# Kernel optimization log

Hardware: AMD Instinct MI355X
Metric: run time of the kernel (lower is better)

The kernel has to match this reference:

```python
import jax, jax.numpy as jnp
import numpy as np

B_, N, C, H = 512, 49, 256, 8
DH = C // H            # 32
RB, NRF = 8, 32
NWIN = B_ // RB        # 64
DC = 64                # class_token_dim
TC = C + 2 * DC        # 384
WS = 7
SCALE = DH ** -0.5


def _rel_pos_index():
    ch = np.arange(WS)
    coords = np.stack(np.meshgrid(ch, ch, indexing='ij')).reshape(2, -1)  # [2,49]
    rel = (coords[:, :, None] - coords[:, None, :]).transpose(1, 2, 0)    # [49,49,2]
    rel[..., 0] += WS - 1
    rel[..., 1] += WS - 1
    rel[..., 0] *= 2 * WS - 1
    return jnp.asarray(rel.sum(-1).reshape(-1))  # [49*49]


def _ln(x, axes, eps=1e-5):
    m = x.mean(axes, keepdims=True)
    v = x.var(axes, keepdims=True)
    return (x - m) * jax.lax.rsqrt(v + eps)


def setup_inputs() -> dict:
    key = jax.random.key(0)
    ks = jax.random.split(key, 20)
    def w(i, shape, s=0.02):
        return jax.random.normal(ks[i], shape, jnp.float32) * s
    return dict(
        x=w(0, (B_, N, C), 1.0),
        x_ref=w(1, (RB, NRF, C), 1.0),
        depth_token=w(2, (B_, N, DC), 1.0),
        seg_token=w(3, (B_, N, DC), 1.0),
        qkv_w=w(4, (C, 3 * C)), qkv_b=jnp.zeros(3 * C, jnp.float32),
        proj_w=w(5, (C, C)), proj_b=jnp.zeros(C, jnp.float32),
        rel_bias=w(6, ((2 * WS - 1) ** 2, H)),
        diff_mu=w(7, (1, 1, C), 1.0), diff_logsigma=w(8, (1, 1, C)),
        ref_qk_w=w(9, (C, 2 * C)), ref_qk_b=jnp.zeros(2 * C, jnp.float32),
        conv_w=w(10, (H, H, 3, 3), 0.1), conv_b=jnp.zeros(H, jnp.float32),
        q_norm_w=jnp.ones(C, jnp.float32), q_norm_b=jnp.zeros(C, jnp.float32),
        q_proj_w=w(11, (C, C)), q_proj_b=jnp.zeros(C, jnp.float32),
        cls_dth_q_w=w(12, (DC, DC)), cls_dth_q_b=jnp.zeros(DC, jnp.float32),
        cls_seg_q_w=w(13, (DC, DC)), cls_seg_q_b=jnp.zeros(DC, jnp.float32),
        global_k_w=w(14, (TC, TC)), global_k_b=jnp.zeros(TC, jnp.float32),
        global_v_w=w(15, (TC, TC)), global_v_b=jnp.zeros(TC, jnp.float32),
        proj_dth_w=w(16, (DC, DC)), proj_dth_b=jnp.zeros(DC, jnp.float32),
    )


def reference(x, x_ref, depth_token, seg_token, qkv_w, qkv_b, proj_w, proj_b,
              rel_bias, diff_mu, diff_logsigma, ref_qk_w, ref_qk_b, conv_w, conv_b,
              q_norm_w, q_norm_b, q_proj_w, q_proj_b, cls_dth_q_w, cls_dth_q_b,
              cls_seg_q_w, cls_seg_q_b, global_k_w, global_k_b, global_v_w,
              global_v_b, proj_dth_w, proj_dth_b):
    # qkv: [B_,N,3C] -> q,k,v each [B_,H,N,DH]
    qkv = (x @ qkv_w + qkv_b).reshape(B_, N, 3, H, DH).transpose(2, 0, 3, 1, 4)
    q, k, v = qkv[0], qkv[1], qkv[2]

    # ---- group attention (ref branch) ----
    ref_qk = (x_ref @ ref_qk_w + ref_qk_b).reshape(RB, NRF, 2, C).transpose(2, 0, 1, 3)
    ref_q, ref_v = ref_qk[0], ref_qk[1]                       # [RB,NRF,C]
    ref_q = diff_mu + jnp.exp(diff_logsigma) * ref_q
    ref_q = ref_q.reshape(RB, NRF, H, DH).transpose(0, 2, 1, 3)  # [RB,H,NRF,DH]
    ref_v = ref_v.reshape(RB, NRF, H, DH).transpose(0, 2, 1, 3)

    qs = (q * SCALE).reshape(RB, NWIN, H, N, DH)
    # scores against shared (per-image) ref keys; avoids materializing repeated K
    ref_attn = jnp.einsum('rwhnd,rhfd->rhwnf', qs, ref_q)     # [RB,H,NWIN,N,NRF]
    ref_attn_r = ref_attn.reshape(RB, H, NWIN * N, NRF)
    # 3-step diffusion: conv2d over heads-as-channels + LN(no affine) + gelu, residual
    for _ in range(3):
        u = jax.lax.conv_general_dilated(
            ref_attn_r, conv_w, (1, 1), 'SAME',
            dimension_numbers=('NCHW', 'OIHW', 'NCHW')) + conv_b[None, :, None, None]
        u = jax.nn.gelu(_ln(u, (-2, -1)), approximate=False)
        ref_attn_r = ref_attn_r + u
    ref_attn = jax.nn.softmax(ref_attn_r.reshape(RB, H, NWIN, N, NRF), axis=-1)
    q_new = jnp.einsum('rhwnf,rhfd->rwnhd', ref_attn, ref_v).reshape(B_, N, C)
    q_sc = q.transpose(0, 2, 1, 3).reshape(B_, N, C)          # unscaled shortcut
    q_new = (_ln(q_new + q_sc, (-1,)) * q_norm_w + q_norm_b) @ q_proj_w + q_proj_b + q_sc
    q_new = q_new.reshape(B_, N, H, DH).transpose(0, 2, 1, 3) * SCALE

    # ---- window attention with relative position bias ----
    bias = rel_bias[_rel_pos_index()].reshape(N, N, H).transpose(2, 0, 1)  # [H,N,N]
    attn = jax.nn.softmax(jnp.einsum('bhnd,bhmd->bhnm', q_new, k) + bias[None], axis=-1)
    out = jnp.einsum('bhnm,bhmd->bnhd', attn, v).reshape(B_, N, C)
    out = out @ proj_w + proj_b

    # ---- class-token global attention ----
    dch = DC // H   # 8
    tdh = TC // H   # 48
    depth_q = (depth_token @ cls_dth_q_w + cls_dth_q_b).reshape(B_, N, H, dch).transpose(0, 2, 1, 3) * SCALE
    seg_q = (seg_token @ cls_seg_q_w + cls_seg_q_b).reshape(B_, N, H, dch).transpose(0, 2, 1, 3) * SCALE
    t_x = jnp.concatenate([out, depth_token, seg_token], axis=-1)  # [B_,N,TC]
    t_k = (t_x @ global_k_w + global_k_b).reshape(B_, N, H, tdh).transpose(0, 2, 1, 3)
    t_v = (t_x @ global_v_w + global_v_b).reshape(B_, N, H, tdh).transpose(0, 2, 1, 3)

    d_attn = jax.nn.softmax(jnp.einsum('bhnc,bhnt->bhct', depth_q, t_k), axis=-1)
    d_tok = jnp.einsum('bhct,bhnt->bhcn', d_attn, t_v).reshape(B_, DC, N).transpose(0, 2, 1)
    d_tok = d_tok @ proj_dth_w + proj_dth_b
    s_attn = jax.nn.softmax(jnp.einsum('bhnc,bhnt->bhct', seg_q, t_k), axis=-1)
    s_tok = jnp.einsum('bhct,bhnt->bhcn', s_attn, t_v).reshape(B_, DC, N).transpose(0, 2, 1)
    s_tok = s_tok @ proj_dth_w + proj_dth_b  # NOTE: original uses proj_dth for seg too
    return out, d_tok, s_tok
```

## Files before the change

kernel.cpp:

```cpp
#include <hip/hip_runtime.h>
#include <hip/hip_bf16.h>

typedef __hip_bfloat16 bf16;
typedef short s16x8 __attribute__((ext_vector_type(8)));
typedef float f32x4 __attribute__((ext_vector_type(4)));
union V16 { uint4 u4; s16x8 s8; unsigned u[4]; unsigned short s[8]; };

static __device__ __forceinline__ float b2f(bf16 v){ return __bfloat162float(v); }
static __device__ __forceinline__ bf16  f2b(float v){ return __float2bfloat16(v); }
static __device__ __forceinline__ unsigned short f2bs(float x){
    union { float f; unsigned u; } c; c.f = x;
    unsigned r = c.u + 0x7fff + ((c.u >> 16) & 1);
    return (unsigned short)(r >> 16);
}
static __device__ __forceinline__ float bu2f(unsigned short b){
    union { unsigned u; float f; } c; c.u = ((unsigned)b) << 16; return c.f;
}
static __device__ __forceinline__ s16x8 ld16g(const bf16* p){
    V16 u; u.u4 = *(const uint4*)p; return u.s8;
}
static __device__ __forceinline__ void glds16(const void* g, void* l){
    __builtin_amdgcn_global_load_lds(
        (const __attribute__((address_space(1))) unsigned*)g,
        (__attribute__((address_space(3))) unsigned*)l, 16, 0, 0);
}

#define SCALE_T 0.17677669529663687f

__global__ __launch_bounds__(256) void prep_weights(
    const float* __restrict__ qkvw, const float* __restrict__ qpw,
    const float* __restrict__ pw,   const float* __restrict__ gkw,
    const float* __restrict__ gvw,  bf16* __restrict__ Wt)
{
    int idx = blockIdx.x * 256 + threadIdx.x;
    float v;
    if (idx < 196608)      { int j = idx;          int n = j >> 8, k = j & 255; v = qkvw[k * 768 + n]; }
    else if (idx < 262144) { int j = idx - 196608; int n = j >> 8, k = j & 255; v = qpw[k * 256 + n]; }
    else if (idx < 327680) { int j = idx - 262144; int n = j >> 8, k = j & 255; v = pw[k * 256 + n]; }
    else if (idx < 475136) { int j = idx - 327680; int n = j / 384, k = j - n * 384; v = gkw[k * 384 + n]; }
    else                   { int j = idx - 475136; int n = j / 384, k = j - n * 384; v = gvw[k * 384 + n]; }
    ((unsigned short*)Wt)[idx] = f2bs(v);
}

__global__ __launch_bounds__(256, 2) void gemm128(
    const void* __restrict__ A, int akind, int lda,
    const float* __restrict__ tokD, const float* __restrict__ tokS,
    const bf16* __restrict__ Wt, const float* __restrict__ bias,
    const float* __restrict__ bias2,
    const bf16* __restrict__ addp, int addStride,
    float* __restrict__ outF, bf16* __restrict__ outB, int outStrideB,
    int M, int K, int N, float scale)
{
    __shared__ char lds[2][16384];

    const int tid = threadIdx.x;
    const int wv = tid >> 6, lane = tid & 63;
    const int quad = lane >> 4, l15 = lane & 15;
    const int wr = wv >> 1, wc = wv & 1;

    const int gx = (int)gridDim.x;
    const int nwg = gx * (int)gridDim.y;
    int bid = (int)blockIdx.y * gx + (int)blockIdx.x;
    if ((nwg & 7) == 0) bid = (bid & 7) * (nwg >> 3) + (bid >> 3);
    const int bx = bid % gx, by = bid / gx;
    const int rowBase = by * 128, colBase = bx * 128;

    const int srow = tid >> 2;
    const int kOff = (((tid & 3) ^ (srow & 3)) << 3);

    const unsigned swz = (unsigned)((quad ^ (l15 & 3)) << 4);
    const unsigned aoff0 = (unsigned)(wr * 4096 + l15 * 64) + swz;
    const unsigned boff0 = (unsigned)(wc * 4096 + l15 * 64) + swz;

    f32x4 acc[4][4];
    #pragma unroll
    for (int m = 0; m < 4; ++m)
        #pragma unroll
        for (int n = 0; n < 4; ++n)
            #pragma unroll
            for (int r = 0; r < 4; ++r) acc[m][n][r] = 0.f;

    const bf16*  Ab = (const bf16*)A;
    const float* Af = (const float*)A;

    auto stage = [&](int sbuf, int kt) {
        char* base = &lds[sbuf][0];
        #pragma unroll
        for (int c = 0; c < 2; ++c) {
            const bf16* src = Wt + (size_t)(colBase + c * 64 + srow) * K + (kt + kOff);
            glds16(src, base + 8192 + c * 4096 + tid * 16);
        }
        if (akind == 0) {
            #pragma unroll
            for (int c = 0; c < 2; ++c) {
                const bf16* src = Ab + (size_t)(rowBase + c * 64 + srow) * lda + (kt + kOff);
                glds16(src, base + c * 4096 + tid * 16);
            }
        } else {
            #pragma unroll
            for (int c = 0; c < 2; ++c) {
                int row = rowBase + c * 64 + srow;
                const float* src;
                if (akind == 1) {
                    src = Af + (size_t)row * lda + (kt + kOff);
                } else {
                    if (kt < 256)      src = Af   + (size_t)row * 256 + (kt + kOff);
                    else if (kt < 320) src = tokD + (size_t)row * 64  + (kt - 256 + kOff);
                    else               src = tokS + (size_t)row * 64  + (kt - 320 + kOff);
                }
                float4 u0 = ((const float4*)src)[0];
                float4 u1 = ((const float4*)src)[1];
                V16 o;
                o.s[0] = f2bs(u0.x); o.s[1] = f2bs(u0.y);
                o.s[2] = f2bs(u0.z); o.s[3] = f2bs(u0.w);
                o.s[4] = f2bs(u1.x); o.s[5] = f2bs(u1.y);
                o.s[6] = f2bs(u1.z); o.s[7] = f2bs(u1.w);
                *(uint4*)(base + c * 4096 + tid * 16) = o.u4;
            }
        }
    };

    stage(0, 0);
    __syncthreads();
    int buf = 0;
    for (int kt = 0; kt < K; kt += 32) {
        if (kt + 32 < K) stage(buf ^ 1, kt + 32);
        const char* Abase = &lds[buf][0];
        const char* Bbase = Abase + 8192;
        s16x8 af[4], bfr[4];
        #pragma unroll
        for (int m = 0; m < 4; ++m) af[m]  = *(const s16x8*)(Abase + aoff0 + m * 1024);
        #pragma unroll
        for (int n = 0; n < 4; ++n) bfr[n] = *(const s16x8*)(Bbase + boff0 + n * 1024);
        #pragma unroll
        for (int m = 0; m < 4; ++m)
            #pragma unroll
            for (int n = 0; n < 4; ++n)
                acc[m][n] = __builtin_amdgcn_mfma_f32_16x16x32_bf16(af[m], bfr[n], acc[m][n], 0, 0, 0);
        __syncthreads();
        buf ^= 1;
    }

    #pragma unroll
    for (int n = 0; n < 4; ++n) {
        int col = colBase + wc * 64 + n * 16 + l15;
        float bb = bias2 ? (col < 384 ? bias[col] : bias2[col - 384]) : bias[col];
        #pragma unroll
        for (int m = 0; m < 4; ++m) {
            #pragma unroll
            for (int r = 0; r < 4; ++r) {
                int row = rowBase + wr * 64 + m * 16 + quad * 4 + r;
                float v = acc[m][n][r] + bb;
                if (addp) v += b2f(addp[(size_t)row * addStride + col]);
                v *= scale;
                if (outF) outF[(size_t)row * N + col] = v;
                if (outB) outB[(size_t)row * outStrideB + col] = f2b(v);
            }
        }
    }
}

__global__ __launch_bounds__(256) void mfma_gemm(
    const void* __restrict__ A, int a_mode,
    const float* __restrict__ Xd, const float* __restrict__ Xs,
    const float* __restrict__ W, const float* __restrict__ bias,
    const bf16* __restrict__ addp, int addStride,
    float* __restrict__ outF, bf16* __restrict__ outB,
    int M, int K, int N, float scale)
{
    __shared__ __hip_bfloat16 Al[64][48];
    __shared__ __hip_bfloat16 Bl[64][48];

    const int tid  = threadIdx.x;
    const int wv   = tid >> 6, lane = tid & 63;
    const int quad = lane >> 4, l15 = lane & 15;
    const int rowBase = blockIdx.y * 64, colBase = blockIdx.x * 64;

    const int am = tid >> 2, ak = (tid & 3) * 8;
    const int bn = tid & 63, bk = (tid >> 6) * 8;

    f32x4 acc[4];
    #pragma unroll
    for (int t = 0; t < 4; ++t)
        #pragma unroll
        for (int r = 0; r < 4; ++r) acc[t][r] = 0.f;

    for (int kt = 0; kt < K; kt += 32) {
        s16x8 sa;
        if (a_mode == 1) {
            const bf16* Ab = (const bf16*)A;
            V16 u; u.u4 = *(const uint4*)(Ab + (size_t)(rowBase + am) * K + kt + ak);
            sa = u.s8;
        } else {
            const float* src; size_t base;
            if (a_mode == 0) {
                src = (const float*)A; base = (size_t)(rowBase + am) * K + kt + ak;
            } else {
                int kcol = kt + ak;
                if (kcol < 256)      { src = (const float*)A; base = (size_t)(rowBase + am) * 256 + kcol; }
                else if (kcol < 320) { src = Xd; base = (size_t)(rowBase + am) * 64 + (kcol - 256); }
                else                 { src = Xs; base = (size_t)(rowBase + am) * 64 + (kcol - 320); }
            }
            const float4* p = (const float4*)(src + base);
            float4 u0 = p[0], u1 = p[1];
            sa[0] = (short)f2bs(u0.x); sa[1] = (short)f2bs(u0.y);
            sa[2] = (short)f2bs(u0.z); sa[3] = (short)f2bs(u0.w);
            sa[4] = (short)f2bs(u1.x); sa[5] = (short)f2bs(u1.y);
            sa[6] = (short)f2bs(u1.z); sa[7] = (short)f2bs(u1.w);
        }
        *(s16x8*)&Al[am][ak] = sa;

        s16x8 sb;
        #pragma unroll
        for (int j = 0; j < 8; ++j)
            sb[j] = (short)f2bs(W[(size_t)(kt + bk + j) * N + colBase + bn]);
        *(s16x8*)&Bl[bn][bk] = sb;

        __syncthreads();

        s16x8 a = *(const s16x8*)&Al[wv * 16 + l15][quad * 8];
        #pragma unroll
        for (int t = 0; t < 4; ++t) {
            s16x8 b = *(const s16x8*)&Bl[t * 16 + l15][quad * 8];
            acc[t] = __builtin_amdgcn_mfma_f32_16x16x32_bf16(a, b, acc[t], 0, 0, 0);
        }
        __syncthreads();
    }

    #pragma unroll
    for (int t = 0; t < 4; ++t) {
        int col = colBase + t * 16 + l15;
        float bb = bias[col];
        #pragma unroll
        for (int r = 0; r < 4; ++r) {
            int row = rowBase + wv * 16 + quad * 4 + r;
            float v = acc[t][r] + bb;
            if (addp) v += b2f(addp[(size_t)row * addStride + col]);
            v *= scale;
            if (outF) outF[(size_t)row * N + col] = v;
            if (outB) outB[(size_t)row * N + col] = f2b(v);
        }
    }
}

__global__ __launch_bounds__(256) void refprep_kernel(
    const float* __restrict__ ref_qk, const float* __restrict__ mu,
    const float* __restrict__ ls, float* __restrict__ ref_q_t,
    float* __restrict__ ref_v_t)
{
    int idx = blockIdx.x * 256 + threadIdx.x;
    int d = idx & 31, f = (idx >> 5) & 31, h = (idx >> 10) & 7, r = idx >> 13;
    int c = h * 32 + d;
    size_t src = (size_t)(r * 32 + f) * 512 + c;
    ref_q_t[idx] = mu[c] + __expf(ls[c]) * ref_qk[src];
    ref_v_t[idx] = ref_qk[src + 256];
}

__global__ __launch_bounds__(256) void refattn_kernel(
    const bf16* __restrict__ qkv, const float* __restrict__ ref_q_t,
    bf16* __restrict__ ref_attn)
{
    int blk = blockIdx.x;
    int w = blk & 63, h = (blk >> 6) & 7, r = blk >> 9;
    int b = r * 64 + w;
    __shared__ float qt[49 * 32];
    __shared__ float rq[32 * 33];
    int tid = threadIdx.x;
    for (int l = tid; l < 1568; l += 256) {
        int n = l >> 5, d = l & 31;
        qt[l] = b2f(qkv[(size_t)(b * 49 + n) * 768 + h * 32 + d]) * SCALE_T;
    }
    for (int l = tid; l < 1024; l += 256) {
        int f = l >> 5, d = l & 31;
        rq[f * 33 + d] = ref_q_t[(size_t)((r * 8 + h) * 32 + f) * 32 + d];
    }
    __syncthreads();
    for (int l = tid; l < 1568; l += 256) {
        int n = l >> 5, f = l & 31;
        float acc = 0.f;
        #pragma unroll
        for (int d2 = 0; d2 < 32; ++d2) acc += qt[n * 32 + d2] * rq[f * 33 + d2];
        ref_attn[(size_t)(((r * 8 + h) * 64 + w) * 49 + n) * 32 + f] = f2b(acc);
    }
}

__global__ __launch_bounds__(256) void conv_kernel(
    const bf16* __restrict__ in, const float* __restrict__ conv_w,
    const float* __restrict__ conv_b, bf16* __restrict__ u)
{
    __shared__ float w_s[576];
    __shared__ float b_s[8];
    int tid = threadIdx.x;
    for (int l = tid; l < 576; l += 256) w_s[l] = conv_w[l];
    if (tid < 8) b_s[tid] = conv_b[tid];
    __syncthreads();

    int idx = blockIdx.x * 256 + tid;
    int fb = idx & 3;
    int p  = (idx >> 2) % 3136;
    int r  = idx / 12544;
    int f0 = fb * 8;

    float acc[8][8];
    #pragma unroll
    for (int o = 0; o < 8; ++o) {
        float bo = b_s[o];
        #pragma unroll
        for (int f = 0; f < 8; ++f) acc[o][f] = bo;
    }

    for (int i = 0; i < 8; ++i) {
        float ext[3][10];
        #pragma unroll
        for (int dy = 0; dy < 3; ++dy) {
            int pp = p + dy - 1;
            bool pv = (unsigned)pp < 3136u;
            size_t base = ((size_t)((r * 8 + i) * 3136 + (pv ? pp : 0))) * 32 + f0;
            V16 uv;
            uv.u4 = pv ? *(const uint4*)(in + base) : make_uint4(0, 0, 0, 0);
            #pragma unroll
            for (int j = 0; j < 8; ++j) {
                unsigned sh = uv.u[j >> 1];
                unsigned bits = (j & 1) ? (sh & 0xffff0000u) : (sh << 16);
                union { unsigned uu; float fl; } cv; cv.uu = bits;
                ext[dy][j + 1] = cv.fl;
            }
            ext[dy][0] = (pv && f0 > 0)      ? b2f(in[base - 1]) : 0.f;
            ext[dy][9] = (pv && f0 + 8 < 32) ? b2f(in[base + 8]) : 0.f;
        }
        #pragma unroll
        for (int o = 0; o < 8; ++o) {
            #pragma unroll
            for (int ky = 0; ky < 3; ++ky) {
                const float* wp = &w_s[((o * 8 + i) * 3 + ky) * 3];
                float w0 = wp[0], w1 = wp[1], w2 = wp[2];
                #pragma unroll
                for (int f = 0; f < 8; ++f)
                    acc[o][f] += ext[ky][f] * w0 + ext[ky][f + 1] * w1 + ext[ky][f + 2] * w2;
            }
        }
    }

    #pragma unroll
    for (int o = 0; o < 8; ++o) {
        bf16 ov[8];
        #pragma unroll
        for (int f = 0; f < 8; ++f) ov[f] = f2b(acc[o][f]);
        *(uint4*)(u + ((size_t)((r * 8 + o) * 3136 + p)) * 32 + f0) = *(uint4*)ov;
    }
}

__global__ __launch_bounds__(256) void lnstats_kernel(
    const bf16* __restrict__ u, float* __restrict__ stats)
{
    int g = blockIdx.x;
    const bf16* p = u + (size_t)g * 100352;
    int tid = threadIdx.x;
    float s = 0.f, s2 = 0.f;
    for (int it = tid; it < 12544; it += 256) {
        V16 uv; uv.u4 = *(const uint4*)(p + it * 8);
        #pragma unroll
        for (int j = 0; j < 8; ++j) {
            unsigned sh = uv.u[j >> 1];
            unsigned bits = (j & 1) ? (sh & 0xffff0000u) : (sh << 16);
            union { unsigned uu; float fl; } cv; cv.uu = bits;
            s += cv.fl; s2 += cv.fl * cv.fl;
        }
    }
    __shared__ float r1[256], r2[256];
    r1[tid] = s; r2[tid] = s2; __syncthreads();
    for (int st = 128; st > 0; st >>= 1) {
        if (tid < st) { r1[tid] += r1[tid + st]; r2[tid] += r2[tid + st]; }
        __syncthreads();
    }
    if (tid == 0) {
        float mean = r1[0] * (1.f / 100352.f);
        float var  = r2[0] * (1.f / 100352.f) - mean * mean;
        var = fmaxf(var, 0.f);
        stats[g * 2] = mean;
        stats[g * 2 + 1] = rsqrtf(var + 1e-5f);
    }
}

__global__ __launch_bounds__(256) void lngelu_kernel(
    const bf16* __restrict__ u, const float* __restrict__ stats,
    bf16* __restrict__ ref_attn)
{
    int idx8 = blockIdx.x * 256 + threadIdx.x;
    int g = idx8 / 12544;
    size_t base = (size_t)idx8 * 8;
    float mean = stats[g * 2], rstd = stats[g * 2 + 1];
    V16 uv; uv.u4 = *(const uint4*)(u + base);
    V16 rv; rv.u4 = *(const uint4*)(ref_attn + base);
    bf16 outv[8];
    #pragma unroll
    for (int j = 0; j < 8; ++j) {
        unsigned shu = uv.u[j >> 1];
        unsigned shr = rv.u[j >> 1];
        unsigned bu = (j & 1) ? (shu & 0xffff0000u) : (shu << 16);
        unsigned br = (j & 1) ? (shr & 0xffff0000u) : (shr << 16);
        union { unsigned uu; float fl; } cu, cr; cu.uu = bu; cr.uu = br;
        float v = (cu.fl - mean) * rstd;
        float ge = 0.5f * v * (1.f + erff(v * 0.7071067811865476f));
        outv[j] = f2b(cr.fl + ge);
    }
    *(uint4*)(ref_attn + base) = *(uint4*)outv;
}

__global__ __launch_bounds__(256) void qnew_pre_kernel(
    const bf16* __restrict__ qkv, const bf16* __restrict__ ref_attn,
    const float* __restrict__ ref_v_t,
    const float* __restrict__ qnw, const float* __restrict__ qnb,
    bf16* __restrict__ ln_t)
{
    int ww = threadIdx.x >> 6, lane = threadIdx.x & 63;
    int row = blockIdx.x * 4 + ww;
    int b = row / 49, n = row % 49;
    int r = b >> 6, w = b & 63;
    int h = lane >> 3, d0 = (lane & 7) * 4;

    const bf16* la = ref_attn + ((size_t)(((r * 8 + h) * 64 + w) * 49 + n)) * 32 + d0;
    ushort4 lu = *(const ushort4*)la;
    float lg[4] = { bu2f(lu.x), bu2f(lu.y), bu2f(lu.z), bu2f(lu.w) };

    float m = fmaxf(fmaxf(lg[0], lg[1]), fmaxf(lg[2], lg[3]));
    m = fmaxf(m, __shfl_xor(m, 1));
    m = fmaxf(m, __shfl_xor(m, 2));
    m = fmaxf(m, __shfl_xor(m, 4));
    float p[4], s = 0.f;
    #pragma unroll
    for (int j = 0; j < 4; ++j) { p[j] = __expf(lg[j] - m); s += p[j]; }
    s += __shfl_xor(s, 1);
    s += __shfl_xor(s, 2);
    s += __shfl_xor(s, 4);
    float inv = 1.f / s;
    #pragma unroll
    for (int j = 0; j < 4; ++j) p[j] *= inv;

    const float* rv = ref_v_t + ((size_t)(r * 8 + h) * 32) * 32 + d0;
    float y[4] = {0.f, 0.f, 0.f, 0.f};
    #pragma unroll
    for (int f = 0; f < 32; ++f) {
        int src = (lane & 56) | (f >> 2);
        float pf = __shfl(p[f & 3], src);
        float4 rvf = *(const float4*)(rv + f * 32);
        y[0] += pf * rvf.x; y[1] += pf * rvf.y;
        y[2] += pf * rvf.z; y[3] += pf * rvf.w;
    }

    ushort4 qu = *(const ushort4*)(qkv + (size_t)row * 768 + lane * 4);
    float z[4] = { y[0] + bu2f(qu.x), y[1] + bu2f(qu.y),
                   y[2] + bu2f(qu.z), y[3] + bu2f(qu.w) };

    float s1 = z[0] + z[1] + z[2] + z[3];
    #pragma unroll
    for (int off = 1; off < 64; off <<= 1) s1 += __shfl_xor(s1, off);
    float mean = s1 * (1.f / 256.f);
    float zc[4] = { z[0] - mean, z[1] - mean, z[2] - mean, z[3] - mean };
    float s2 = zc[0]*zc[0] + zc[1]*zc[1] + zc[2]*zc[2] + zc[3]*zc[3];
    #pragma unroll
    for (int off = 1; off < 64; off <<= 1) s2 += __shfl_xor(s2, off);
    float rstd = rsqrtf(s2 * (1.f / 256.f) + 1e-5f);

    float4 wv = *(const float4*)(qnw + lane * 4);
    float4 bv = *(const float4*)(qnb + lane * 4);
    bf16 outv[4];
    outv[0] = f2b(zc[0] * rstd * wv.x + bv.x);
    outv[1] = f2b(zc[1] * rstd * wv.y + bv.y);
    outv[2] = f2b(zc[2] * rstd * wv.z + bv.z);
    outv[3] = f2b(zc[3] * rstd * wv.w + bv.w);
    *(ushort4*)(ln_t + (size_t)row * 256 + lane * 4) = *(ushort4*)outv;
}

__global__ __launch_bounds__(256) void winattn_kernel(
    const bf16* __restrict__ qkv, const bf16* __restrict__ q_new,
    const float* __restrict__ rel_bias, bf16* __restrict__ attn_out)
{
    const int wv = threadIdx.x >> 6, lane = threadIdx.x & 63;
    const int quad = lane >> 4, l15 = lane & 15;
    const int b = blockIdx.x >> 1;
    const int h = (blockIdx.x & 1) * 4 + wv;

    __shared__ bf16 lds[4 * 6912];
    bf16* P  = &lds[wv * 6912];
    bf16* vT = P + 4608;

    {
        int m = lane;
        if (m < 49) {
            const bf16* vp = qkv + ((size_t)(b * 49 + m)) * 768 + 512 + h * 32;
            V16 v0, v1, v2, v3;
            v0.u4 = *(const uint4*)(vp);
            v1.u4 = *(const uint4*)(vp + 8);
            v2.u4 = *(const uint4*)(vp + 16);
            v3.u4 = *(const uint4*)(vp + 24);
            #pragma unroll
            for (int d = 0; d < 8; ++d) {
                ((unsigned short*)vT)[d * 72 + m]        = v0.s[d];
                ((unsigned short*)vT)[(d + 8) * 72 + m]  = v1.s[d];
                ((unsigned short*)vT)[(d + 16) * 72 + m] = v2.s[d];
                ((unsigned short*)vT)[(d + 24) * 72 + m] = v3.s[d];
            }
        } else {
            #pragma unroll
            for (int d = 0; d < 32; ++d)
                ((unsigned short*)vT)[d * 72 + m] = 0;
        }
    }

    s16x8 aq[4], bk[4];
    #pragma unroll
    for (int t = 0; t < 4; ++t) {
        int qr = t * 16 + l15; qr = qr > 48 ? 48 : qr;
        aq[t] = ld16g(q_new + ((size_t)(b * 49 + qr)) * 256 + h * 32 + quad * 8);
        bk[t] = ld16g(qkv + ((size_t)(b * 49 + qr)) * 768 + 256 + h * 32 + quad * 8);
    }
    f32x4 S[4][4];
    #pragma unroll
    for (int tn = 0; tn < 4; ++tn)
        #pragma unroll
        for (int tm = 0; tm < 4; ++tm) {
            #pragma unroll
            for (int r = 0; r < 4; ++r) S[tn][tm][r] = 0.f;
            S[tn][tm] = __builtin_amdgcn_mfma_f32_16x16x32_bf16(aq[tn], bk[tm], S[tn][tm], 0, 0, 0);
        }

    int mvalid[4], mi[4], mj[4];
    #pragma unroll
    for (int tm = 0; tm < 4; ++tm) {
        int m0 = tm * 16 + l15;
        mvalid[tm] = (m0 < 49);
        int mc = m0 > 48 ? 48 : m0;
        mi[tm] = mc / 7; mj[tm] = mc - mi[tm] * 7;
    }
    #pragma unroll
    for (int tn = 0; tn < 4; ++tn) {
        #pragma unroll
        for (int r = 0; r < 4; ++r) {
            int n0 = tn * 16 + quad * 4 + r;
            int nc = n0 > 48 ? 48 : n0;
            int ni = nc / 7, nj = nc - (nc / 7) * 7;
            float vals[4];
            float mx = -1e30f;
            #pragma unroll
            for (int tm = 0; tm < 4; ++tm) {
                float v = S[tn][tm][r]
                        + rel_bias[((ni - mi[tm] + 6) * 13 + (nj - mj[tm] + 6)) * 8 + h];
                if (!mvalid[tm]) v = -1e30f;
                vals[tm] = v;
                mx = fmaxf(mx, v);
            }
            mx = fmaxf(mx, __shfl_xor(mx, 1));
            mx = fmaxf(mx, __shfl_xor(mx, 2));
            mx = fmaxf(mx, __shfl_xor(mx, 4));
            mx = fmaxf(mx, __shfl_xor(mx, 8));
            float s = 0.f;
            #pragma unroll
            for (int tm = 0; tm < 4; ++tm) { vals[tm] = __expf(vals[tm] - mx); s += vals[tm]; }
            s += __shfl_xor(s, 1);
            s += __shfl_xor(s, 2);
            s += __shfl_xor(s, 4);
            s += __shfl_xor(s, 8);
            float inv = 1.f / s;
            #pragma unroll
            for (int tm = 0; tm < 4; ++tm)
                ((unsigned short*)P)[n0 * 72 + tm * 16 + l15] = f2bs(vals[tm] * inv);
        }
    }

    f32x4 O[4][2];
    #pragma unroll
    for (int tn = 0; tn < 4; ++tn)
        #pragma unroll
        for (int td = 0; td < 2; ++td)
            #pragma unroll
            for (int r = 0; r < 4; ++r) O[tn][td][r] = 0.f;

    #pragma unroll
    for (int ks = 0; ks < 2; ++ks) {
        s16x8 bv0 = *(const s16x8*)&vT[(0 * 16 + l15) * 72 + ks * 32 + quad * 8];
        s16x8 bv1 = *(const s16x8*)&vT[(1 * 16 + l15) * 72 + ks * 32 + quad * 8];
        #pragma unroll
        for (int tn = 0; tn < 4; ++tn) {
            s16x8 ap = *(const s16x8*)&P[(tn * 16 + l15) * 72 + ks * 32 + quad * 8];
            O[tn][0] = __builtin_amdgcn_mfma_f32_16x16x32_bf16(ap, bv0, O[tn][0], 0, 0, 0);
            O[tn][1] = __builtin_amdgcn_mfma_f32_16x16x32_bf16(ap, bv1, O[tn][1], 0, 0, 0);
        }
    }

    #pragma unroll
    for (int tn = 0; tn < 4; ++tn)
        #pragma unroll
        for (int r = 0; r < 4; ++r) {
            int n0 = tn * 16 + quad * 4 + r;
            if (n0 < 49) {
                size_t base = ((size_t)(b * 49 + n0)) * 256 + h * 32;
                attn_out[base + l15]      = f2b(O[tn][0][r]);
                attn_out[base + 16 + l15] = f2b(O[tn][1][r]);
            }
        }
}

__global__ __launch_bounds__(256) void clsattn_kernel(
    const bf16* __restrict__ tkv,
    const bf16* __restrict__ depth_q, const bf16* __restrict__ seg_q,
    bf16* __restrict__ d_pre, bf16* __restrict__ s_pre)
{
    const int wv = threadIdx.x >> 6, lane = threadIdx.x & 63;
    const int quad = lane >> 4, l15 = lane & 15;
    const int bh = blockIdx.x * 4 + wv;
    const int b = bh >> 3, h = bh & 7;

    __shared__ bf16 lds[4 * 5760];
    unsigned short* QP = (unsigned short*)&lds[wv * 5760];
    unsigned short* KV = QP + 1152;

    {
        int n = lane;
        V16 dv, sv;
        if (n < 49) {
            dv.u4 = *(const uint4*)(depth_q + ((size_t)(b * 49 + n)) * 64 + h * 8);
            sv.u4 = *(const uint4*)(seg_q   + ((size_t)(b * 49 + n)) * 64 + h * 8);
        } else {
            dv.u4 = make_uint4(0, 0, 0, 0); sv.u4 = make_uint4(0, 0, 0, 0);
        }
        #pragma unroll
        for (int c = 0; c < 8; ++c) {
            QP[c * 72 + n]       = dv.s[c];
            QP[(8 + c) * 72 + n] = sv.s[c];
        }
    }
    {
        int n = lane;
        V16 k[6];
        if (n < 49) {
            const bf16* kp = tkv + ((size_t)(b * 49 + n)) * 768 + h * 48;
            #pragma unroll
            for (int c6 = 0; c6 < 6; ++c6) k[c6].u4 = *(const uint4*)(kp + c6 * 8);
        } else {
            #pragma unroll
            for (int c6 = 0; c6 < 6; ++c6) k[c6].u4 = make_uint4(0, 0, 0, 0);
        }
        #pragma unroll
        for (int c6 = 0; c6 < 6; ++c6)
            #pragma unroll
            for (int j = 0; j < 8; ++j)
                KV[(c6 * 8 + j) * 72 + n] = k[c6].s[j];
    }

    f32x4 S[3];
    #pragma unroll
    for (int t3 = 0; t3 < 3; ++t3)
        #pragma unroll
        for (int r = 0; r < 4; ++r) S[t3][r] = 0.f;
    #pragma unroll
    for (int ks = 0; ks < 2; ++ks) {
        s16x8 a = *(const s16x8*)&QP[l15 * 72 + ks * 32 + quad * 8];
        #pragma unroll
        for (int t3 = 0; t3 < 3; ++t3) {
            s16x8 bf = *(const s16x8*)&KV[(t3 * 16 + l15) * 72 + ks * 32 + quad * 8];
            S[t3] = __builtin_amdgcn_mfma_f32_16x16x32_bf16(a, bf, S[t3], 0, 0, 0);
        }
    }

    #pragma unroll
    for (int r = 0; r < 4; ++r) {
        float v0 = S[0][r], v1 = S[1][r], v2 = S[2][r];
        float mx = fmaxf(fmaxf(v0, v1), v2);
        mx = fmaxf(mx, __shfl_xor(mx, 1));
        mx = fmaxf(mx, __shfl_xor(mx, 2));
        mx = fmaxf(mx, __shfl_xor(mx, 4));
        mx = fmaxf(mx, __shfl_xor(mx, 8));
        float e0 = __expf(v0 - mx), e1 = __expf(v1 - mx), e2 = __expf(v2 - mx);
        float s = e0 + e1 + e2;
        s += __shfl_xor(s, 1);
        s += __shfl_xor(s, 2);
        s += __shfl_xor(s, 4);
        s += __shfl_xor(s, 8);
        float inv = 1.f / s;
        int c = quad * 4 + r;
        QP[c * 72 + 0 * 16 + l15] = f2bs(e0 * inv);
        QP[c * 72 + 1 * 16 + l15] = f2bs(e1 * inv);
        QP[c * 72 + 2 * 16 + l15] = f2bs(e2 * inv);
    }
    #pragma unroll
    for (int z = 0; z < 4; ++z)
        QP[(lane & 15) * 72 + 48 + (lane >> 4) * 4 + z] = 0;

    {
        int n = lane;
        V16 v[6], zv; zv.u4 = make_uint4(0, 0, 0, 0);
        if (n < 49) {
            const bf16* vp = tkv + ((size_t)(b * 49 + n)) * 768 + 384 + h * 48;
            #pragma unroll
            for (int c6 = 0; c6 < 6; ++c6) v[c6].u4 = *(const uint4*)(vp + c6 * 8);
        } else {
            #pragma unroll
            for (int c6 = 0; c6 < 6; ++c6) v[c6].u4 = zv.u4;
        }
        #pragma unroll
        for (int c6 = 0; c6 < 6; ++c6)
            *(uint4*)&KV[n * 72 + c6 * 8] = v[c6].u4;
        *(uint4*)&KV[n * 72 + 48] = zv.u4;
        *(uint4*)&KV[n * 72 + 56] = zv.u4;
    }

    f32x4 O[4];
    #pragma unroll
    for (int t4 = 0; t4 < 4; ++t4)
        #pragma unroll
        for (int r = 0; r < 4; ++r) O[t4][r] = 0.f;
    #pragma unroll
    for (int ks = 0; ks < 2; ++ks) {
        s16x8 a = *(const s16x8*)&QP[l15 * 72 + ks * 32 + quad * 8];
        #pragma unroll
        for (int t4 = 0; t4 < 4; ++t4) {
            s16x8 bf = *(const s16x8*)&KV[(t4 * 16 + l15) * 72 + ks * 32 + quad * 8];
            O[t4] = __builtin_amdgcn_mfma_f32_16x16x32_bf16(a, bf, O[t4], 0, 0, 0);
        }
    }

    #pragma unroll
    for (int t4 = 0; t4 < 4; ++t4) {
        int n = t4 * 16 + l15;
        if (n < 49) {
            size_t base = ((size_t)(b * 49 + n)) * 64 + h * 8;
            #pragma unroll
            for (int r = 0; r < 4; ++r) {
                int c = quad * 4 + r;
                if (c < 8) d_pre[base + c] = f2b(O[t4][r]);
                else       s_pre[base + c - 8] = f2b(O[t4][r]);
            }
        }
    }
}

extern "C" void kernel_launch(void* const* d_in, const int* in_sizes, int n_in,
                              void* d_out, int out_size, void* d_ws, size_t ws_size,
                              hipStream_t stream)
{
    const float* x          = (const float*)d_in[0];
    const float* x_ref      = (const float*)d_in[1];
    const float* dth_tok    = (const float*)d_in[2];
    const float* seg_tok    = (const float*)d_in[3];
    const float* qkv_w      = (const float*)d_in[4];
    const float* qkv_b      = (const float*)d_in[5];
    const float* proj_w     = (const float*)d_in[6];
    const float* proj_b     = (const float*)d_in[7];
    const float* rel_bias   = (const float*)d_in[8];
    const float* diff_mu    = (const float*)d_in[9];
    const float* diff_ls    = (const float*)d_in[10];
    const float* ref_qk_w   = (const float*)d_in[11];
    const float* ref_qk_b   = (const float*)d_in[12];
    const float* conv_w     = (const float*)d_in[13];
    const float* conv_b     = (const float*)d_in[14];
    const float* q_norm_w   = (const float*)d_in[15];
    const float* q_norm_b   = (const float*)d_in[16];
    const float* q_proj_w   = (const float*)d_in[17];
    const float* q_proj_b   = (const float*)d_in[18];
    const float* cls_dth_w  = (const float*)d_in[19];
    const float* cls_dth_b  = (const float*)d_in[20];
    const float* cls_seg_w  = (const float*)d_in[21];
    const float* cls_seg_b  = (const float*)d_in[22];
    const float* glob_k_w   = (const float*)d_in[23];
    const float* glob_k_b   = (const float*)d_in[24];
    const float* glob_v_w   = (const float*)d_in[25];
    const float* glob_v_b   = (const float*)d_in[26];
    const float* proj_dth_w = (const float*)d_in[27];
    const float* proj_dth_b = (const float*)d_in[28];

    bf16* wsb = (bf16*)d_ws;
    bf16* qkv      = wsb;
    bf16* tkv      = wsb;
    bf16* ref_attn = wsb + 19267584;
    bf16* q_new    = ref_attn;
    bf16* depth_q  = ref_attn;
    bf16* seg_q    = ref_attn + 1605632;
    bf16* d_pre    = ref_attn + 3211264;
    bf16* s_pre    = ref_attn + 4816896;
    bf16* u_buf    = wsb + 25690112;
    bf16* ln_t     = u_buf;
    bf16* attn_out = u_buf;
    float* ref_qk  = (float*)((char*)d_ws + 64225280);
    float* ref_q_t = ref_qk + 131072;
    float* ref_v_t = ref_q_t + 65536;
    float* stats   = ref_v_t + 65536;

    float* out0  = (float*)d_out;
    float* out_d = out0 + 6422528;
    float* out_s = out0 + 8028160;

    bf16* Wt_all = (bf16*)out_d;

    prep_weights<<<2432, 256, 0, stream>>>(qkv_w, q_proj_w, proj_w, glob_k_w, glob_v_w, Wt_all);

    gemm128<<<dim3(6, 196), 256, 0, stream>>>(x, 1, 256, nullptr, nullptr,
        Wt_all, qkv_b, nullptr, nullptr, 0, nullptr, qkv, 768, 25088, 256, 768, 1.f);
    mfma_gemm<<<dim3(8, 4), 256, 0, stream>>>(x_ref, 0, nullptr, nullptr, ref_qk_w, ref_qk_b,
                                              nullptr, 0, ref_qk, nullptr, 256, 256, 512, 1.f);
    refprep_kernel<<<256, 256, 0, stream>>>(ref_qk, diff_mu, diff_ls, ref_q_t, ref_v_t);
    refattn_kernel<<<4096, 256, 0, stream>>>(qkv, ref_q_t, ref_attn);
    for (int it = 0; it < 3; ++it) {
        conv_kernel<<<392, 256, 0, stream>>>(ref_attn, conv_w, conv_b, u_buf);
        lnstats_kernel<<<64, 256, 0, stream>>>(u_buf, stats);
        lngelu_kernel<<<3136, 256, 0, stream>>>(u_buf, stats, ref_attn);
    }
    qnew_pre_kernel<<<6272, 256, 0, stream>>>(qkv, ref_attn, ref_v_t,
                                              q_norm_w, q_norm_b, ln_t);
    gemm128<<<dim3(2, 196), 256, 0, stream>>>(ln_t, 0, 256, nullptr, nullptr,
        Wt_all + 196608, q_proj_b, nullptr, qkv, 768, nullptr, q_new, 256, 25088, 256, 256, SCALE_T);
    winattn_kernel<<<1024, 256, 0, stream>>>(qkv, q_new, rel_bias, attn_out);
    gemm128<<<dim3(2, 196), 256, 0, stream>>>(attn_out, 0, 256, nullptr, nullptr,
        Wt_all + 262144, proj_b, nullptr, nullptr, 0, out0, nullptr, 0, 25088, 256, 256, 1.f);
    gemm128<<<dim3(6, 196), 256, 0, stream>>>(out0, 2, 256, dth_tok, seg_tok,
        Wt_all + 327680, glob_k_b, glob_v_b, nullptr, 0, nullptr, tkv, 768, 25088, 384, 768, 1.f);
    mfma_gemm<<<dim3(1, 392), 256, 0, stream>>>(dth_tok, 0, nullptr, nullptr, cls_dth_w, cls_dth_b,
                                                nullptr, 0, nullptr, depth_q, 25088, 64, 64, SCALE_T);
    mfma_gemm<<<dim3(1, 392), 256, 0, stream>>>(seg_tok, 0, nullptr, nullptr, cls_seg_w, cls_seg_b,
                                                nullptr, 0, nullptr, seg_q, 25088, 64, 64, SCALE_T);
    clsattn_kernel<<<1024, 256, 0, stream>>>(tkv, depth_q, seg_q, d_pre, s_pre);
    mfma_gemm<<<dim3(1, 392), 256, 0, stream>>>(d_pre, 1, nullptr, nullptr, proj_dth_w, proj_dth_b,
                                                nullptr, 0, out_d, nullptr, 25088, 64, 64, 1.f);
    mfma_gemm<<<dim3(1, 392), 256, 0, stream>>>(s_pre, 1, nullptr, nullptr, proj_dth_w, proj_dth_b,
                                                nullptr, 0, out_s, nullptr, 25088, 64, 64, 1.f);
}
```

Measured before the change: 561.2 us.

## Pre-convert GEMM inputs to bf16, stage bf16 outputs through LDS, split LN stats

Adds a standalone fp32-to-bf16 conversion of x so the QKV GEMM loads A with async global-to-LDS copies. The proj GEMM now also writes a bf16 copy of its output, which the global K/V GEMM consumes directly; only the token part is still converted inline. bf16 epilogue stores go through a swizzled LDS tile so each thread writes 16-byte coalesced chunks. The LDS swizzle is changed, occupancy is raised to 4 blocks per CU, and LayerNorm statistics are split across 4x more blocks, with the partial sums combined in the GELU kernel. The trade-off is an extra conversion pass and an extra bf16 output buffer.

Measured after the change: 494.0 us. -12.0%, faster.

```diff
diff --git a/kernel.cpp b/kernel.cpp
--- a/kernel.cpp
+++ b/kernel.cpp
@@ -42,14 +42,25 @@
     ((unsigned short*)Wt)[idx] = f2bs(v);
 }
 
-__global__ __launch_bounds__(256, 2) void gemm128(
-    const void* __restrict__ A, int akind, int lda,
+__global__ __launch_bounds__(256) void convert_f32_bf16(
+    const float* __restrict__ in, bf16* __restrict__ out)
+{
+    int i = blockIdx.x * 256 + threadIdx.x;
+    float4 v = ((const float4*)in)[i];
+    ushort4 o;
+    o.x = f2bs(v.x); o.y = f2bs(v.y); o.z = f2bs(v.z); o.w = f2bs(v.w);
+    ((ushort4*)out)[i] = o;
+}
+
+template<int TOK>
+__global__ __launch_bounds__(256, 4) void gemm_bb(
+    const bf16* __restrict__ A, int lda,
     const float* __restrict__ tokD, const float* __restrict__ tokS,
     const bf16* __restrict__ Wt, const float* __restrict__ bias,
     const float* __restrict__ bias2,
     const bf16* __restrict__ addp, int addStride,
     float* __restrict__ outF, bf16* __restrict__ outB, int outStrideB,
-    int M, int K, int N, float scale)
+    int K, int N, float scale)
 {
     __shared__ char lds[2][16384];
 
@@ -66,9 +77,9 @@
     const int rowBase = by * 128, colBase = bx * 128;
 
     const int srow = tid >> 2;
-    const int kOff = (((tid & 3) ^ (srow & 3)) << 3);
-
-    const unsigned swz = (unsigned)((quad ^ (l15 & 3)) << 4);
+    const int kOffE = (((tid & 3) ^ ((srow >> 1) & 3)) << 3);
+
+    const unsigned swz = (unsigned)((quad ^ ((l15 >> 1) & 3)) << 4);
     const unsigned aoff0 = (unsigned)(wr * 4096 + l15 * 64) + swz;
     const unsigned boff0 = (unsigned)(wc * 4096 + l15 * 64) + swz;
 
@@ -80,36 +91,26 @@
             #pragma unroll
             for (int r = 0; r < 4; ++r) acc[m][n][r] = 0.f;
 
-    const bf16*  Ab = (const bf16*)A;
-    const float* Af = (const float*)A;
-
     auto stage = [&](int sbuf, int kt) {
         char* base = &lds[sbuf][0];
         #pragma unroll
-        for (int c = 0; c < 2; ++c) {
-            const bf16* src = Wt + (size_t)(colBase + c * 64 + srow) * K + (kt + kOff);
-            glds16(src, base + 8192 + c * 4096 + tid * 16);
-        }
-        if (akind == 0) {
-            #pragma unroll
-            for (int c = 0; c < 2; ++c) {
-                const bf16* src = Ab + (size_t)(rowBase + c * 64 + srow) * lda + (kt + kOff);
-                glds16(src, base + c * 4096 + tid * 16);
-            }
+        for (int c = 0; c < 2; ++c)
+            glds16(Wt + (size_t)(colBase + c * 64 + srow) * K + (kt + kOffE),
+                   base + 8192 + c * 4096 + tid * 16);
+        if (!TOK || kt < 256) {
+            #pragma unroll
+            for (int c = 0; c < 2; ++c)
+                glds16(A + (size_t)(rowBase + c * 64 + srow) * lda + (kt + kOffE),
+                       base + c * 4096 + tid * 16);
         } else {
             #pragma unroll
             for (int c = 0; c < 2; ++c) {
                 int row = rowBase + c * 64 + srow;
-                const float* src;
-                if (akind == 1) {
-                    src = Af + (size_t)row * lda + (kt + kOff);
-                } else {
-                    if (kt < 256)      src = Af   + (size_t)row * 256 + (kt + kOff);
-                    else if (kt < 320) src = tokD + (size_t)row * 64  + (kt - 256 + kOff);
-                    else               src = tokS + (size_t)row * 64  + (kt - 320 + kOff);
-                }
-                float4 u0 = ((const float4*)src)[0];
-                float4 u1 = ((const float4*)src)[1];
+                const float* sf = (kt < 320)
+                    ? (tokD + (size_t)row * 64 + (kt - 256 + kOffE))
+                    : (tokS + (size_t)row * 64 + (kt - 320 + kOffE));
+                float4 u0 = ((const float4*)sf)[0];
+                float4 u1 = ((const float4*)sf)[1];
                 V16 o;
                 o.s[0] = f2bs(u0.x); o.s[1] = f2bs(u0.y);
                 o.s[2] = f2bs(u0.z); o.s[3] = f2bs(u0.w);
@@ -125,13 +126,13 @@
     int buf = 0;
     for (int kt = 0; kt < K; kt += 32) {
         if (kt + 32 < K) stage(buf ^ 1, kt + 32);
-        const char* Abase = &lds[buf][0];
-        const char* Bbase = Abase + 8192;
+        const char* Ab2 = &lds[buf][0];
+        const char* Bb2 = Ab2 + 8192;
         s16x8 af[4], bfr[4];
         #pragma unroll
-        for (int m = 0; m < 4; ++m) af[m]  = *(const s16x8*)(Abase + aoff0 + m * 1024);
-        #pragma unroll
-        for (int n = 0; n < 4; ++n) bfr[n] = *(const s16x8*)(Bbase + boff0 + n * 1024);
+        for (int m = 0; m < 4; ++m) af[m]  = *(const s16x8*)(Ab2 + aoff0 + m * 1024);
+        #pragma unroll
+        for (int n = 0; n < 4; ++n) bfr[n] = *(const s16x8*)(Bb2 + boff0 + n * 1024);
         #pragma unroll
         for (int m = 0; m < 4; ++m)
             #pragma unroll
@@ -141,20 +142,50 @@
         buf ^= 1;
     }
 
-    #pragma unroll
-    for (int n = 0; n < 4; ++n) {
-        int col = colBase + wc * 64 + n * 16 + l15;
-        float bb = bias2 ? (col < 384 ? bias[col] : bias2[col - 384]) : bias[col];
-        #pragma unroll
-        for (int m = 0; m < 4; ++m) {
-            #pragma unroll
-            for (int r = 0; r < 4; ++r) {
-                int row = rowBase + wr * 64 + m * 16 + quad * 4 + r;
-                float v = acc[m][n][r] + bb;
-                if (addp) v += b2f(addp[(size_t)row * addStride + col]);
-                v *= scale;
-                if (outF) outF[(size_t)row * N + col] = v;
-                if (outB) outB[(size_t)row * outStrideB + col] = f2b(v);
+    if (outB) {
+        #pragma unroll
+        for (int n = 0; n < 4; ++n) {
+            int col = colBase + wc * 64 + n * 16 + l15;
+            float bb = bias2 ? (col < 384 ? bias[col] : bias2[col - 384]) : bias[col];
+            #pragma unroll
+            for (int m = 0; m < 4; ++m) {
+                #pragma unroll
+                for (int r = 0; r < 4; ++r) {
+                    int rl = wr * 64 + m * 16 + quad * 4 + r;
+                    float v = acc[m][n][r] + bb;
+                    if (addp) v += b2f(addp[(size_t)(rowBase + rl) * addStride + col]);
+                    v *= scale;
+                    if (outF) outF[(size_t)(rowBase + rl) * N + col] = v;
+                    int cbyte = (wc * 64 + n * 16 + l15) * 2;
+                    int blk = ((cbyte >> 5) ^ ((rl >> 2) & 7)) & 7;
+                    *(unsigned short*)((char*)lds + rl * 256 + (blk << 5) + (cbyte & 31)) = f2bs(v);
+                }
+            }
+        }
+        __syncthreads();
+        #pragma unroll
+        for (int i = 0; i < 8; ++i) {
+            int lin = i * 256 + tid;
+            int rl = lin >> 4, cb = lin & 15;
+            int cb2 = ((((cb >> 1) ^ ((rl >> 2) & 7)) & 7) << 1) | (cb & 1);
+            uint4 val = *(const uint4*)((const char*)lds + rl * 256 + cb2 * 16);
+            *(uint4*)(outB + (size_t)(rowBase + rl) * outStrideB + colBase + cb * 8) = val;
+        }
+    } else {
+        #pragma unroll
+        for (int n = 0; n < 4; ++n) {
+            int col = colBase + wc * 64 + n * 16 + l15;
+            float bb = bias2 ? (col < 384 ? bias[col] : bias2[col - 384]) : bias[col];
+            #pragma unroll
+            for (int m = 0; m < 4; ++m) {
+                #pragma unroll
+                for (int r = 0; r < 4; ++r) {
+                    int rl = wr * 64 + m * 16 + quad * 4 + r;
+                    float v = acc[m][n][r] + bb;
+                    if (addp) v += b2f(addp[(size_t)(rowBase + rl) * addStride + col]);
+                    v *= scale;
+                    if (outF) outF[(size_t)(rowBase + rl) * N + col] = v;
+                }
             }
         }
     }
@@ -351,13 +382,13 @@
 }
 
 __global__ __launch_bounds__(256) void lnstats_kernel(
-    const bf16* __restrict__ u, float* __restrict__ stats)
-{
-    int g = blockIdx.x;
-    const bf16* p = u + (size_t)g * 100352;
+    const bf16* __restrict__ u, float* __restrict__ stats4)
+{
+    int g4 = blockIdx.x;
+    const bf16* p = u + (size_t)g4 * 25088;
     int tid = threadIdx.x;
     float s = 0.f, s2 = 0.f;
-    for (int it = tid; it < 12544; it += 256) {
+    for (int it = tid; it < 3136; it += 256) {
         V16 uv; uv.u4 = *(const uint4*)(p + it * 8);
         #pragma unroll
         for (int j = 0; j < 8; ++j) {
@@ -374,22 +405,28 @@
         __syncthreads();
     }
     if (tid == 0) {
-        float mean = r1[0] * (1.f / 100352.f);
-        float var  = r2[0] * (1.f / 100352.f) - mean * mean;
-        var = fmaxf(var, 0.f);
-        stats[g * 2] = mean;
-        stats[g * 2 + 1] = rsqrtf(var + 1e-5f);
+        stats4[g4 * 2]     = r1[0];
+        stats4[g4 * 2 + 1] = r2[0];
     }
 }
 
 __global__ __launch_bounds__(256) void lngelu_kernel(
-    const bf16* __restrict__ u, const float* __restrict__ stats,
+    const bf16* __restrict__ u, const float* __restrict__ stats4,
     bf16* __restrict__ ref_attn)
 {
     int idx8 = blockIdx.x * 256 + threadIdx.x;
     int g = idx8 / 12544;
     size_t base = (size_t)idx8 * 8;
-    float mean = stats[g * 2], rstd = stats[g * 2 + 1];
+    float sum = 0.f, sq = 0.f;
+    #pragma unroll
+    for (int q = 0; q < 4; ++q) {
+        sum += stats4[(g * 4 + q) * 2];
+        sq  += stats4[(g * 4 + q) * 2 + 1];
+    }
+    float mean = sum * (1.f / 100352.f);
+    float var  = sq * (1.f / 100352.f) - mean * mean;
+    var = fmaxf(var, 0.f);
+    float rstd = rsqrtf(var + 1e-5f);
     V16 uv; uv.u4 = *(const uint4*)(u + base);
     V16 rv; rv.u4 = *(const uint4*)(ref_attn + base);
     bf16 outv[8];
@@ -774,17 +811,19 @@
     bf16* tkv      = wsb;
     bf16* ref_attn = wsb + 19267584;
     bf16* q_new    = ref_attn;
+    bf16* out0b    = ref_attn;
     bf16* depth_q  = ref_attn;
     bf16* seg_q    = ref_attn + 1605632;
     bf16* d_pre    = ref_attn + 3211264;
     bf16* s_pre    = ref_attn + 4816896;
     bf16* u_buf    = wsb + 25690112;
+    bf16* xb       = u_buf;
     bf16* ln_t     = u_buf;
     bf16* attn_out = u_buf;
     float* ref_qk  = (float*)((char*)d_ws + 64225280);
     float* ref_q_t = ref_qk + 131072;
     float* ref_v_t = ref_q_t + 65536;
-    float* stats   = ref_v_t + 65536;
+    float* stats4  = ref_qk;
 
     float* out0  = (float*)d_out;
     float* out_d = out0 + 6422528;
@@ -793,27 +832,28 @@
     bf16* Wt_all = (bf16*)out_d;
 
     prep_weights<<<2432, 256, 0, stream>>>(qkv_w, q_proj_w, proj_w, glob_k_w, glob_v_w, Wt_all);
-
-    gemm128<<<dim3(6, 196), 256, 0, stream>>>(x, 1, 256, nullptr, nullptr,
-        Wt_all, qkv_b, nullptr, nullptr, 0, nullptr, qkv, 768, 25088, 256, 768, 1.f);
+    convert_f32_bf16<<<6272, 256, 0, stream>>>(x, xb);
+
+    gemm_bb<0><<<dim3(6, 196), 256, 0, stream>>>(xb, 256, nullptr, nullptr,
+        Wt_all, qkv_b, nullptr, nullptr, 0, nullptr, qkv, 768, 256, 768, 1.f);
     mfma_gemm<<<dim3(8, 4), 256, 0, stream>>>(x_ref, 0, nullptr, nullptr, ref_qk_w, ref_qk_b,
                                               nullptr, 0, ref_qk, nullptr, 256, 256, 512, 1.f);
     refprep_kernel<<<256, 256, 0, stream>>>(ref_qk, diff_mu, diff_ls, ref_q_t, ref_v_t);
     refattn_kernel<<<4096, 256, 0, stream>>>(qkv, ref_q_t, ref_attn);
     for (int it = 0; it < 3; ++it) {
         conv_kernel<<<392, 256, 0, stream>>>(ref_attn, conv_w, conv_b, u_buf);
-        lnstats_kernel<<<64, 256, 0, stream>>>(u_buf, stats);
-        lngelu_kernel<<<3136, 256, 0, stream>>>(u_buf, stats, ref_attn);
+        lnstats_kernel<<<256, 256, 0, stream>>>(u_buf, stats4);
+        lngelu_kernel<<<3136, 256, 0, stream>>>(u_buf, stats4, ref_attn);
     }
     qnew_pre_kernel<<<6272, 256, 0, stream>>>(qkv, ref_attn, ref_v_t,
                                               q_norm_w, q_norm_b, ln_t);
-    gemm128<<<dim3(2, 196), 256, 0, stream>>>(ln_t, 0, 256, nullptr, nullptr,
-        Wt_all + 196608, q_proj_b, nullptr, qkv, 768, nullptr, q_new, 256, 25088, 256, 256, SCALE_T);
+    gemm_bb<0><<<dim3(2, 196), 256, 0, stream>>>(ln_t, 256, nullptr, nullptr,
+        Wt_all + 196608, q_proj_b, nullptr, qkv, 768, nullptr, q_new, 256, 256, 256, SCALE_T);
     winattn_kernel<<<1024, 256, 0, stream>>>(qkv, q_new, rel_bias, attn_out);
-    gemm128<<<dim3(2, 196), 256, 0, stream>>>(attn_out, 0, 256, nullptr, nullptr,
-        Wt_all + 262144, proj_b, nullptr, nullptr, 0, out0, nullptr, 0, 25088, 256, 256, 1.f);
-    gemm128<<<dim3(6, 196), 256, 0, stream>>>(out0, 2, 256, dth_tok, seg_tok,
-        Wt_all + 327680, glob_k_b, glob_v_b, nullptr, 0, nullptr, tkv, 768, 25088, 384, 768, 1.f);
+    gemm_bb<0><<<dim3(2, 196), 256, 0, stream>>>(attn_out, 256, nullptr, nullptr,
+        Wt_all + 262144, proj_b, nullptr, nullptr, 0, out0, out0b, 256, 256, 256, 1.f);
+    gemm_bb<1><<<dim3(6, 196), 256, 0, stream>>>(out0b, 256, dth_tok, seg_tok,
+        Wt_all + 327680, glob_k_b, glob_v_b, nullptr, 0, nullptr, tkv, 768, 384, 768, 1.f);
     mfma_gemm<<<dim3(1, 392), 256, 0, stream>>>(dth_tok, 0, nullptr, nullptr, cls_dth_w, cls_dth_b,
                                                 nullptr, 0, nullptr, depth_q, 25088, 64, 64, SCALE_T);
     mfma_gemm<<<dim3(1, 392), 256, 0, stream>>>(seg_tok, 0, nullptr, nullptr, cls_seg_w, cls_seg_b,
```
